# Kernel optimization log

Measured on AMD Instinct MI355X. Metric: run time of the kernel, lower is better.

## Reference

```python
import jax, jax.numpy as jnp
import numpy as np

HIDDEN = 1024
BETA = 1.0
SPARSITY_THRESHOLD = 1.0


def _sparsemax(x):
    # Faithful port of the module's custom sparsemax (including its
    # nonstandard per-position tau). Operates over the last axis.
    n = x.shape[-1]
    z = x - jnp.max(x, axis=-1, keepdims=True)
    sum_z = jnp.sum(z, axis=-1, keepdims=True)
    step = (sum_z - 1.0) / n                       # step_size
    sorted_z = -jnp.sort(-z, axis=-1)              # descending sort
    cumsum_z = jnp.cumsum(sorted_z, axis=-1)
    is_gt = sorted_z > step
    rng = jnp.arange(1, n + 1, dtype=jnp.int32)
    k = jnp.max(rng * is_gt, axis=-1, keepdims=True).astype(x.dtype)
    tau = (cumsum_z - 1.0 - step * k) / k          # [.., n] per-position tau
    return jnp.clip(z - tau, 0.0)


def setup_inputs() -> dict:
    key = jax.random.key(0)
    kx, kq, kk, kv = jax.random.split(key, 4)
    B, S, D = 4, 2048, 1024
    x = jax.random.normal(kx, (B, S, D), dtype=jnp.float32)
    # torch Linear weight layout: [out_features, in_features]
    scale = 1.0 / np.sqrt(D)
    Wq = jax.random.normal(kq, (HIDDEN, D), dtype=jnp.float32) * scale
    Wk = jax.random.normal(kk, (HIDDEN, D), dtype=jnp.float32) * scale
    Wv = jax.random.normal(kv, (HIDDEN, D), dtype=jnp.float32) * scale
    return {"x": x, "Wq": Wq, "Wk": Wk, "Wv": Wv}


def reference(x, Wq, Wk, Wv):
    Q = jnp.einsum('bsd,hd->bsh', x, Wq)
    K = jnp.einsum('bsd,hd->bsh', x, Wk)
    V = jnp.einsum('bsd,hd->bsh', x, Wv)
    energy = jnp.einsum('bsh,bth->bst', Q, K) / jnp.sqrt(jnp.asarray(HIDDEN, x.dtype))
    scores = energy * BETA
    sparsity = jnp.mean(jnp.abs(x))
    attention = jax.lax.cond(
        sparsity < SPARSITY_THRESHOLD,
        _sparsemax,
        lambda s: jax.nn.softmax(s, axis=-1),
        scores,
    )
    return jnp.einsum('bst,bth->bsh', attention, V)
```

## Files before the change

kernel.cpp:

```cpp
#include <hip/hip_runtime.h>
#include <math.h>

#define B_   4
#define S_   2048
#define D_   1024
#define H_   1024
#define NROW 2048
#define TOTX 8388608.0f

typedef _Float16 f16x8 __attribute__((ext_vector_type(8)));
typedef float f32x4 __attribute__((ext_vector_type(4)));
typedef unsigned short us8 __attribute__((ext_vector_type(8)));

__device__ __forceinline__ unsigned short f2h(float f) {
  _Float16 h = (_Float16)f;
  return __builtin_bit_cast(unsigned short, h);
}
__device__ __forceinline__ float h2f(unsigned short u) {
  return (float)__builtin_bit_cast(_Float16, u);
}

#define GLD16(gp, lp)                                                            \
  __builtin_amdgcn_global_load_lds(                                              \
      (__attribute__((address_space(1))) void*)(gp),                             \
      (__attribute__((address_space(3))) void*)(lp), 16, 0, 0)

__global__ __launch_bounds__(256) void f2h_abs_kernel(const float* __restrict__ in,
                                                      unsigned short* __restrict__ out,
                                                      float* absOut, int n4) {
  int i0 = blockIdx.x * 256 + threadIdx.x;
  int stride = gridDim.x * 256;
  float s = 0.f;
  for (int i = i0; i < n4; i += stride) {
    float4 v = ((const float4*)in)[i];
    ushort4 o;
    o.x = f2h(v.x); o.y = f2h(v.y); o.z = f2h(v.z); o.w = f2h(v.w);
    ((ushort4*)out)[i] = o;
    s += fabsf(v.x) + fabsf(v.y) + fabsf(v.z) + fabsf(v.w);
  }
#pragma unroll
  for (int off = 32; off; off >>= 1) s += __shfl_xor(s, off);
  __shared__ float red[4];
  if ((threadIdx.x & 63) == 0) red[threadIdx.x >> 6] = s;
  __syncthreads();
  if (threadIdx.x == 0) atomicAdd(absOut, red[0] + red[1] + red[2] + red[3]);
}

__global__ __launch_bounds__(256) void f2h3_kernel(const float* __restrict__ a,
                                                   const float* __restrict__ b,
                                                   const float* __restrict__ c,
                                                   unsigned short* __restrict__ oa,
                                                   unsigned short* __restrict__ ob,
                                                   unsigned short* __restrict__ oc,
                                                   int n4) {
  int i = blockIdx.x * 256 + threadIdx.x;
  if (i >= n4) return;
  const float* in = (blockIdx.y == 0) ? a : (blockIdx.y == 1) ? b : c;
  unsigned short* out = (blockIdx.y == 0) ? oa : (blockIdx.y == 1) ? ob : oc;
  float4 v = ((const float4*)in)[i];
  ushort4 o;
  o.x = f2h(v.x); o.y = f2h(v.y); o.z = f2h(v.z); o.w = f2h(v.w);
  ((ushort4*)out)[i] = o;
}

template <int MI, bool OUT_F16>
__global__ __launch_bounds__(512, 2) void gemm8_nt(const unsigned short* __restrict__ A,
                                                   const unsigned short* __restrict__ B,
                                                   void* __restrict__ Cv,
                                                   unsigned short* __restrict__ VT,
                                                   int M, int N, int K,
                                                   long long sA, long long sB, long long sC,
                                                   float scale) {
  constexpr int BM  = MI * 32;
  constexpr int ASZ = BM * 32;
  constexpr int BSZ = 256 * 32;
  constexpr int TSZ = ASZ + BSZ;

  const int bz = blockIdx.z;
  A += (long long)bz * sA;
  B += (long long)bz * sB;

  __shared__ __align__(16) unsigned short lds[3 * TSZ];

  const int tid = threadIdx.x;
  const int lane = tid & 63;
  const int w = tid >> 6;
  const int wr = w >> 2;
  const int wc = w & 3;
  const int m0 = blockIdx.y * BM, n0 = blockIdx.x * 256;

  f32x4 acc[MI][4] = {};

  const int srow = tid >> 2;
  const int scol = ((lane & 3) ^ ((lane >> 3) & 3)) * 8;
  const unsigned short* gA0 = A + (long long)(m0 + srow) * K + scol;
  const unsigned short* gA1 = gA0 + (long long)128 * K;
  const unsigned short* gB0 = B + (long long)(n0 + srow) * K + scol;
  const unsigned short* gB1 = gB0 + (long long)128 * K;
  const int wb = w * 512;

  const int fm = lane & 15;
  const int col8 = ((lane >> 4) ^ ((lane >> 1) & 3)) * 8;
  int aoff[MI], boff[4];
#pragma unroll
  for (int mi = 0; mi < MI; ++mi) aoff[mi] = (wr * (MI * 16) + mi * 16 + fm) * 32 + col8;
#pragma unroll
  for (int ni = 0; ni < 4; ++ni) boff[ni] = ASZ + (wc * 64 + ni * 16 + fm) * 32 + col8;

  const int nt = K >> 5;

#define STAGEP(Lp, k0)                                   \
  do {                                                   \
    GLD16(gA0 + (k0), (Lp) + wb);                        \
    if (MI == 8) GLD16(gA1 + (k0), (Lp) + 4096 + wb);    \
    GLD16(gB0 + (k0), (Lp) + ASZ + wb);                  \
    GLD16(gB1 + (k0), (Lp) + ASZ + 4096 + wb);           \
  } while (0)

  unsigned short* L0 = lds;
  unsigned short* L1 = lds + TSZ;
  unsigned short* L2 = lds + 2 * TSZ;

  STAGEP(L0, 0);
  STAGEP(L1, 32);
  if (MI == 8) asm volatile("s_waitcnt vmcnt(4)" ::: "memory");
  else         asm volatile("s_waitcnt vmcnt(3)" ::: "memory");
  __builtin_amdgcn_s_barrier();

  for (int t = 0; t < nt; ++t) {
    f16x8 af[MI], bf[4];
#pragma unroll
    for (int mi = 0; mi < MI; ++mi) af[mi] = *(const f16x8*)(L0 + aoff[mi]);
#pragma unroll
    for (int ni = 0; ni < 4; ++ni) bf[ni] = *(const f16x8*)(L0 + boff[ni]);
    if (t + 2 < nt) STAGEP(L2, (t + 2) << 5);
    asm volatile("s_waitcnt lgkmcnt(0)" ::: "memory");
    __builtin_amdgcn_sched_barrier(0);
    __builtin_amdgcn_s_setprio(1);
#pragma unroll
    for (int mi = 0; mi < MI; ++mi)
#pragma unroll
      for (int ni = 0; ni < 4; ++ni)
        acc[mi][ni] = __builtin_amdgcn_mfma_f32_16x16x32_f16(af[mi], bf[ni],
                                                             acc[mi][ni], 0, 0, 0);
    __builtin_amdgcn_s_setprio(0);
    if (t + 2 < nt) {
      if (MI == 8) asm volatile("s_waitcnt vmcnt(4)" ::: "memory");
      else         asm volatile("s_waitcnt vmcnt(3)" ::: "memory");
    } else if (t + 1 < nt) {
      asm volatile("s_waitcnt vmcnt(0)" ::: "memory");
    }
    __builtin_amdgcn_s_barrier();
    unsigned short* tmp = L0; L0 = L1; L1 = L2; L2 = tmp;
  }
#undef STAGEP

  const int cm = (lane >> 4) * 4;
  const int cn = lane & 15;
  if (VT != nullptr && bz == 2) {
#pragma unroll
    for (int mi = 0; mi < MI; ++mi)
#pragma unroll
      for (int ni = 0; ni < 4; ++ni) {
        int m = m0 + wr * (MI * 16) + mi * 16 + cm;
        int n = n0 + wc * 64 + ni * 16 + cn;
        int b = m >> 11, s = m & 2047;
        ushort4 o;
        o.x = f2h(acc[mi][ni][0] * scale);
        o.y = f2h(acc[mi][ni][1] * scale);
        o.z = f2h(acc[mi][ni][2] * scale);
        o.w = f2h(acc[mi][ni][3] * scale);
        *(ushort4*)(VT + (long long)b * (H_ * S_) + (long long)n * S_ + s) = o;
      }
    return;
  }
#pragma unroll
  for (int mi = 0; mi < MI; ++mi)
#pragma unroll
    for (int ni = 0; ni < 4; ++ni) {
#pragma unroll
      for (int r = 0; r < 4; ++r) {
        long long m = m0 + wr * (MI * 16) + mi * 16 + cm + r;
        long long n = n0 + wc * 64 + ni * 16 + cn;
        float v = acc[mi][ni][r] * scale;
        if (OUT_F16)
          ((unsigned short*)Cv)[(long long)bz * sC + m * N + n] = f2h(v);
        else
          ((float*)Cv)[(long long)bz * sC + m * N + n] = v;
      }
    }
}

template <int K, int J>
__device__ __forceinline__ void intra_s(float (&r)[32]) {
#pragma unroll
  for (int v = 0; v < 32; ++v)
    if ((v & J) == 0) {
      const int u = v | J;
      const bool dsc = ((v & K) == 0);
      float a = r[v], b = r[u];
      float mx = fmaxf(a, b), mn = fminf(a, b);
      r[v] = dsc ? mx : mn;
      r[u] = dsc ? mn : mx;
    }
}

template <int J>
__device__ __forceinline__ void intra_desc(float (&r)[32]) {
#pragma unroll
  for (int v = 0; v < 32; ++v)
    if ((v & J) == 0) {
      const int u = v | J;
      float a = r[v], b = r[u];
      r[v] = fmaxf(a, b);
      r[u] = fminf(a, b);
    }
}

template <int JL>
__device__ __forceinline__ void cross_desc(float (&r)[32], int lane, int bp32) {
  const bool keepmax = ((lane & JL) == 0);
  float b[32];
#pragma unroll
  for (int v = 0; v < 32; ++v) {
    int av = __builtin_bit_cast(int, r[v]);
    int bv;
    if constexpr (JL == 32)
      bv = __builtin_amdgcn_ds_bpermute(bp32, av);
    else
      bv = __builtin_amdgcn_ds_swizzle(av, (JL << 10) | 0x1F);
    b[v] = __builtin_bit_cast(float, bv);
  }
  __builtin_amdgcn_sched_barrier(0);
#pragma unroll
  for (int v = 0; v < 32; ++v) {
    float mx = fmaxf(r[v], b[v]), mn = fminf(r[v], b[v]);
    r[v] = keepmax ? mx : mn;
  }
}

__device__ __forceinline__ void signfix(float (&r)[32], unsigned fix) {
#pragma unroll
  for (int v = 0; v < 32; ++v)
    r[v] = __builtin_bit_cast(float, __builtin_bit_cast(unsigned, r[v]) ^ fix);
}

__global__ __launch_bounds__(256, 4) void attn_row_wave(const unsigned short* __restrict__ scores,
                                                        unsigned short* __restrict__ attn,
                                                        const float* __restrict__ absSum) {
  const int tid = threadIdx.x;
  const int lane = tid & 63;
  const int row = blockIdx.x * 4 + (tid >> 6);
  const unsigned short* rowp = scores + (long long)row * NROW;
  unsigned short* aout = attn + (long long)row * NROW;
  const int bp32 = (lane ^ 32) << 2;

  const us8* rp = (const us8*)(rowp + lane * 32);
  float r[32];
  float lm = -INFINITY, lsraw = 0.f;
#pragma unroll
  for (int q = 0; q < 4; ++q) {
    us8 h = rp[q];
#pragma unroll
    for (int j = 0; j < 8; ++j) {
      float f = h2f((unsigned short)h[j]);
      r[q * 8 + j] = f;
      lm = fmaxf(lm, f);
      lsraw += f;
    }
  }
#pragma unroll
  for (int off = 32; off; off >>= 1) {
    lm = fmaxf(lm, __shfl_xor(lm, off, 64));
    lsraw += __shfl_xor(lsraw, off, 64);
  }

  const bool use_softmax = (absSum[0] * (1.0f / TOTX)) >= 1.0f;

  if (use_softmax) {
    float ls = 0.f;
#pragma unroll
    for (int v = 0; v < 32; ++v) { r[v] = expf(r[v] - lm); ls += r[v]; }
#pragma unroll
    for (int off = 32; off; off >>= 1) ls += __shfl_xor(ls, off, 64);
    float inv = 1.0f / ls;
    us8* op = (us8*)(aout + lane * 32);
#pragma unroll
    for (int q = 0; q < 4; ++q) {
      us8 o;
#pragma unroll
      for (int j = 0; j < 8; ++j) o[j] = f2h(r[q * 8 + j] * inv);
      op[q] = o;
    }
    return;
  }

#pragma unroll
  for (int v = 0; v < 32; ++v) r[v] -= lm;
  const float step = ((lsraw - (float)NROW * lm) - 1.0f) * (1.0f / (float)NROW);

  intra_s<2, 1>(r);
  intra_s<4, 2>(r); intra_s<4, 1>(r);
  intra_s<8, 4>(r); intra_s<8, 2>(r); intra_s<8, 1>(r);
  intra_s<16, 8>(r); intra_s<16, 4>(r); intra_s<16, 2>(r); intra_s<16, 1>(r);

  unsigned cur = (unsigned)(lane & 1) << 31;
  signfix(r, cur);
  intra_desc<16>(r); intra_desc<8>(r); intra_desc<4>(r);
  intra_desc<2>(r); intra_desc<1>(r);

  { unsigned want = (unsigned)(lane & 2) << 30;
    signfix(r, cur ^ want); cur = want; }
  cross_desc<1>(r, lane, bp32);
  intra_desc<16>(r); intra_desc<8>(r); intra_desc<4>(r);
  intra_desc<2>(r); intra_desc<1>(r);

  { unsigned want = (unsigned)(lane & 4) << 29;
    signfix(r, cur ^ want); cur = want; }
  cross_desc<2>(r, lane, bp32); cross_desc<1>(r, lane, bp32);
  intra_desc<16>(r); intra_desc<8>(r); intra_desc<4>(r);
  intra_desc<2>(r); intra_desc<1>(r);

  { unsigned want = (unsigned)(lane & 8) << 28;
    signfix(r, cur ^ want); cur = want; }
  cross_desc<4>(r, lane, bp32); cross_desc<2>(r, lane, bp32);
  cross_desc<1>(r, lane, bp32);
  intra_desc<16>(r); intra_desc<8>(r); intra_desc<4>(r);
  intra_desc<2>(r); intra_desc<1>(r);

  { unsigned want = (unsigned)(lane & 16) << 27;
    signfix(r, cur ^ want); cur = want; }
  cross_desc<8>(r, lane, bp32); cross_desc<4>(r, lane, bp32);
  cross_desc<2>(r, lane, bp32); cross_desc<1>(r, lane, bp32);
  intra_desc<16>(r); intra_desc<8>(r); intra_desc<4>(r);
  intra_desc<2>(r); intra_desc<1>(r);

  { unsigned want = (unsigned)(lane & 32) << 26;
    signfix(r, cur ^ want); cur = want; }
  cross_desc<16>(r, lane, bp32); cross_desc<8>(r, lane, bp32);
  cross_desc<4>(r, lane, bp32); cross_desc<2>(r, lane, bp32);
  cross_desc<1>(r, lane, bp32);
  intra_desc<16>(r); intra_desc<8>(r); intra_desc<4>(r);
  intra_desc<2>(r); intra_desc<1>(r);

  signfix(r, cur);
  cross_desc<32>(r, lane, bp32); cross_desc<16>(r, lane, bp32);
  cross_desc<8>(r, lane, bp32); cross_desc<4>(r, lane, bp32);
  cross_desc<2>(r, lane, bp32); cross_desc<1>(r, lane, bp32);
  intra_desc<16>(r); intra_desc<8>(r); intra_desc<4>(r);
  intra_desc<2>(r); intra_desc<1>(r);

  float lcnt = 0.f;
#pragma unroll
  for (int v = 0; v < 32; ++v) lcnt += (r[v] > step) ? 1.0f : 0.0f;
#pragma unroll
  for (int off = 32; off; off >>= 1) lcnt += __shfl_xor(lcnt, off, 64);
  const float kf = lcnt;

  float run = 0.f;
#pragma unroll
  for (int v = 0; v < 32; ++v) { run += r[v]; r[v] = run; }
  float pre = run;
#pragma unroll
  for (int off = 1; off < 64; off <<= 1) {
    float t = __shfl_up(pre, off, 64);
    if (lane >= off) pre += t;
  }
  pre -= run;
#pragma unroll
  for (int v = 0; v < 32; ++v) r[v] += pre;

  const float inv_k = 1.0f / kf;
  const float c1 = 1.0f + step * kf;

  unsigned long long up = (unsigned long long)rowp;
  asm volatile("" : "+v"(up));
  const us8* rpe = (const us8*)up + lane * 4;
  us8* op = (us8*)(aout + lane * 32);
#pragma unroll
  for (int q = 0; q < 4; ++q) {
    us8 h = rpe[q];
    us8 o;
#pragma unroll
    for (int j = 0; j < 8; ++j) {
      float z = h2f((unsigned short)h[j]) - lm;
      o[j] = f2h(fmaxf(z - (r[q * 8 + j] - c1) * inv_k, 0.0f));
    }
    op[q] = o;
  }
}

extern "C" void kernel_launch(void* const* d_in, const int* in_sizes, int n_in,
                              void* d_out, int out_size, void* d_ws, size_t ws_size,
                              hipStream_t stream) {
  const float* x  = (const float*)d_in[0];
  const float* Wq = (const float*)d_in[1];
  const float* Wk = (const float*)d_in[2];
  const float* Wv = (const float*)d_in[3];
  float* out = (float*)d_out;

  const long long NX = (long long)B_ * S_ * D_;
  const long long NW = (long long)H_ * D_;

  char* base = (char*)d_ws;
  unsigned short* x16  = (unsigned short*)(base);
  unsigned short* Wq16 = (unsigned short*)(base + (16ll << 20));
  unsigned short* Wk16 = (unsigned short*)(base + (18ll << 20));
  unsigned short* Wv16 = (unsigned short*)(base + (20ll << 20));
  unsigned short* Sc16 = (unsigned short*)(base);
  unsigned short* Vt16 = (unsigned short*)(base + (64ll << 20));
  unsigned short* Q16  = (unsigned short*)(base + (80ll << 20));
  unsigned short* K16  = (unsigned short*)(base + (96ll << 20));
  unsigned short* A16  = (unsigned short*)(base + (80ll << 20));
  float*          flag = (float*)(base + (144ll << 20));

  hipMemsetAsync(flag, 0, sizeof(float), stream);

  f2h_abs_kernel<<<1024, 256, 0, stream>>>(x, x16, flag, (int)(NX / 4));
  f2h3_kernel<<<dim3((int)(NW / 4 + 255) / 256, 3), 256, 0, stream>>>(
      Wq, Wk, Wv, Wq16, Wk16, Wv16, (int)(NW / 4));

  {
    dim3 grid(H_ / 256, (B_ * S_) / 128, 3);
    gemm8_nt<4, true><<<grid, 512, 0, stream>>>(x16, Wq16, Q16, Vt16,
                                                B_ * S_, H_, D_,
                                                0, (long long)NW, (long long)(8ll << 20),
                                                1.0f);
  }

  {
    dim3 grid(S_ / 256, S_ / 128, B_);
    gemm8_nt<4, true><<<grid, 512, 0, stream>>>(Q16, K16, Sc16, nullptr,
                                                S_, S_, H_,
                                                (long long)S_ * H_, (long long)S_ * H_,
                                                (long long)S_ * S_, 1.0f / 32.0f);
  }

  attn_row_wave<<<(B_ * S_) / 4, 256, 0, stream>>>(Sc16, A16, flag);

  {
    dim3 grid(H_ / 256, S_ / 128, B_);
    gemm8_nt<4, false><<<grid, 512, 0, stream>>>(A16, Vt16, out, nullptr,
                                                 S_, H_, S_,
                                                 (long long)S_ * S_, (long long)H_ * S_,
                                                 (long long)S_ * H_, 1.0f);
  }
}
```

Measured before the change: 314.3 us.

## Add 256x256-tile ping-pong GEMM kernel for QKV and score GEMMs

Adds a new GEMM kernel that uses 256x256 output tiles (8x4 MFMA fragments per wave) with a triple-buffered LDS pipeline. Each k-step is split into two halves, and the A and B global loads are interleaved between barriers while setprio raises priority around the MFMA blocks. The kernel is used for the QKV projection and the QK^T score GEMM in place of the 128x256 kernel. The aim is more data reuse per tile and better overlap of loads with MFMA, at the cost of one block per CU, higher register pressure and fewer blocks in the grid.

```diff
diff --git a/kernel.cpp b/kernel.cpp
--- a/kernel.cpp
+++ b/kernel.cpp
@@ -63,6 +63,148 @@
   ((ushort4*)out)[i] = o;
 }
 
+template <bool OUT_F16>
+__global__ __launch_bounds__(512, 1) void gemm8p_nt(const unsigned short* __restrict__ A,
+                                                    const unsigned short* __restrict__ B,
+                                                    void* __restrict__ Cv,
+                                                    unsigned short* __restrict__ VT,
+                                                    int M, int N, int K,
+                                                    long long sA, long long sB, long long sC,
+                                                    float scale) {
+  constexpr int ASZ = 256 * 32;
+  constexpr int TSZ = 2 * ASZ;
+
+  const int bz = blockIdx.z;
+  A += (long long)bz * sA;
+  B += (long long)bz * sB;
+
+  __shared__ __align__(16) unsigned short lds[3 * TSZ];
+
+  const int tid = threadIdx.x;
+  const int lane = tid & 63;
+  const int w = tid >> 6;
+  const int wr = w >> 2;
+  const int wc = w & 3;
+  const int m0 = blockIdx.y * 256, n0 = blockIdx.x * 256;
+
+  f32x4 acc[8][4] = {};
+
+  const int srow = tid >> 2;
+  const int scol = ((lane & 3) ^ ((lane >> 3) & 3)) * 8;
+  const unsigned short* gA0 = A + (long long)(m0 + srow) * K + scol;
+  const unsigned short* gA1 = gA0 + (long long)128 * K;
+  const unsigned short* gB0 = B + (long long)(n0 + srow) * K + scol;
+  const unsigned short* gB1 = gB0 + (long long)128 * K;
+  const int wb = w * 512;
+
+  const int fm = lane & 15;
+  const int col8 = ((lane >> 4) ^ ((lane >> 1) & 3)) * 8;
+  int aoff[8], boff[4];
+#pragma unroll
+  for (int mi = 0; mi < 8; ++mi) aoff[mi] = (wr * 128 + mi * 16 + fm) * 32 + col8;
+#pragma unroll
+  for (int ni = 0; ni < 4; ++ni) boff[ni] = ASZ + (wc * 64 + ni * 16 + fm) * 32 + col8;
+
+  const int nt = K >> 5;
+
+#define STAGE4(Lp, k0)                                   \
+  do {                                                   \
+    GLD16(gA0 + (k0), (Lp) + wb);                        \
+    GLD16(gA1 + (k0), (Lp) + 4096 + wb);                 \
+    GLD16(gB0 + (k0), (Lp) + ASZ + wb);                  \
+    GLD16(gB1 + (k0), (Lp) + ASZ + 4096 + wb);           \
+  } while (0)
+
+  unsigned short* L0 = lds;
+  unsigned short* L1 = lds + TSZ;
+  unsigned short* L2 = lds + 2 * TSZ;
+
+  STAGE4(L0, 0);
+  STAGE4(L1, 32);
+  asm volatile("s_waitcnt vmcnt(4)" ::: "memory");
+  __builtin_amdgcn_s_barrier();
+
+  for (int t = 0; t < nt; ++t) {
+    const bool st = (t + 2 < nt);
+    const int k2 = (t + 2) << 5;
+
+    f16x8 af[4], bf[4];
+#pragma unroll
+    for (int mi = 0; mi < 4; ++mi) af[mi] = *(const f16x8*)(L0 + aoff[mi]);
+#pragma unroll
+    for (int ni = 0; ni < 4; ++ni) bf[ni] = *(const f16x8*)(L0 + boff[ni]);
+    if (st) { GLD16(gA0 + k2, L2 + wb); GLD16(gA1 + k2, L2 + 4096 + wb); }
+    __builtin_amdgcn_s_barrier();
+    asm volatile("s_waitcnt lgkmcnt(0)" ::: "memory");
+    __builtin_amdgcn_sched_barrier(0);
+    __builtin_amdgcn_s_setprio(1);
+#pragma unroll
+    for (int mi = 0; mi < 4; ++mi)
+#pragma unroll
+      for (int ni = 0; ni < 4; ++ni)
+        acc[mi][ni] = __builtin_amdgcn_mfma_f32_16x16x32_f16(af[mi], bf[ni],
+                                                             acc[mi][ni], 0, 0, 0);
+    __builtin_amdgcn_s_setprio(0);
+    __builtin_amdgcn_s_barrier();
+
+    f16x8 ag[4];
+#pragma unroll
+    for (int mi = 0; mi < 4; ++mi) ag[mi] = *(const f16x8*)(L0 + aoff[4 + mi]);
+    if (st) { GLD16(gB0 + k2, L2 + ASZ + wb); GLD16(gB1 + k2, L2 + ASZ + 4096 + wb); }
+    __builtin_amdgcn_s_barrier();
+    asm volatile("s_waitcnt lgkmcnt(0)" ::: "memory");
+    __builtin_amdgcn_sched_barrier(0);
+    __builtin_amdgcn_s_setprio(1);
+#pragma unroll
+    for (int mi = 0; mi < 4; ++mi)
+#pragma unroll
+      for (int ni = 0; ni < 4; ++ni)
+        acc[4 + mi][ni] = __builtin_amdgcn_mfma_f32_16x16x32_f16(ag[mi], bf[ni],
+                                                                 acc[4 + mi][ni], 0, 0, 0);
+    __builtin_amdgcn_s_setprio(0);
+    if (st)               asm volatile("s_waitcnt vmcnt(4)" ::: "memory");
+    else if (t + 1 < nt)  asm volatile("s_waitcnt vmcnt(0)" ::: "memory");
+    __builtin_amdgcn_s_barrier();
+    unsigned short* tmp = L0; L0 = L1; L1 = L2; L2 = tmp;
+  }
+#undef STAGE4
+
+  const int cm = (lane >> 4) * 4;
+  const int cn = lane & 15;
+  if (VT != nullptr && bz == 2) {
+#pragma unroll
+    for (int mi = 0; mi < 8; ++mi)
+#pragma unroll
+      for (int ni = 0; ni < 4; ++ni) {
+        int m = m0 + wr * 128 + mi * 16 + cm;
+        int n = n0 + wc * 64 + ni * 16 + cn;
+        int b = m >> 11, s = m & 2047;
+        ushort4 o;
+        o.x = f2h(acc[mi][ni][0] * scale);
+        o.y = f2h(acc[mi][ni][1] * scale);
+        o.z = f2h(acc[mi][ni][2] * scale);
+        o.w = f2h(acc[mi][ni][3] * scale);
+        *(ushort4*)(VT + (long long)b * (H_ * S_) + (long long)n * S_ + s) = o;
+      }
+    return;
+  }
+#pragma unroll
+  for (int mi = 0; mi < 8; ++mi)
+#pragma unroll
+    for (int ni = 0; ni < 4; ++ni) {
+#pragma unroll
+      for (int r = 0; r < 4; ++r) {
+        long long m = m0 + wr * 128 + mi * 16 + cm + r;
+        long long n = n0 + wc * 64 + ni * 16 + cn;
+        float v = acc[mi][ni][r] * scale;
+        if (OUT_F16)
+          ((unsigned short*)Cv)[(long long)bz * sC + m * N + n] = f2h(v);
+        else
+          ((float*)Cv)[(long long)bz * sC + m * N + n] = v;
+      }
+    }
+}
+
 template <int MI, bool OUT_F16>
 __global__ __launch_bounds__(512, 2) void gemm8_nt(const unsigned short* __restrict__ A,
                                                    const unsigned short* __restrict__ B,
@@ -421,19 +563,19 @@
       Wq, Wk, Wv, Wq16, Wk16, Wv16, (int)(NW / 4));
 
   {
-    dim3 grid(H_ / 256, (B_ * S_) / 128, 3);
-    gemm8_nt<4, true><<<grid, 512, 0, stream>>>(x16, Wq16, Q16, Vt16,
-                                                B_ * S_, H_, D_,
-                                                0, (long long)NW, (long long)(8ll << 20),
-                                                1.0f);
+    dim3 grid(H_ / 256, (B_ * S_) / 256, 3);
+    gemm8p_nt<true><<<grid, 512, 0, stream>>>(x16, Wq16, Q16, Vt16,
+                                              B_ * S_, H_, D_,
+                                              0, (long long)NW, (long long)(8ll << 20),
+                                              1.0f);
   }
 
   {
-    dim3 grid(S_ / 256, S_ / 128, B_);
-    gemm8_nt<4, true><<<grid, 512, 0, stream>>>(Q16, K16, Sc16, nullptr,
-                                                S_, S_, H_,
-                                                (long long)S_ * H_, (long long)S_ * H_,
-                                                (long long)S_ * S_, 1.0f / 32.0f);
+    dim3 grid(S_ / 256, S_ / 256, B_);
+    gemm8p_nt<true><<<grid, 512, 0, stream>>>(Q16, K16, Sc16, nullptr,
+                                              S_, S_, H_,
+                                              (long long)S_ * H_, (long long)S_ * H_,
+                                              (long long)S_ * S_, 1.0f / 32.0f);
   }
 
   attn_row_wave<<<(B_ * S_) / 4, 256, 0, stream>>>(Sc16, A16, flag);
```

Result: slower. 324.3 us (+3.2%).
